# Optimization experiments

Measured on AMD Instinct MI355X. Metric: run time of the kernel, lower is better.

Reference implementation:

```python
import jax, jax.numpy as jnp
import numpy as np


def cosine_noise_schedule(t):
    # legacy mode: 1 - cos(t/1.008 * pi/2)^2
    return 1.0 - jnp.cos(t / 1.008 * jnp.pi / 2.0) ** 2


def setup_inputs() -> dict:
    key = jax.random.key(0)
    k1, k2, k3 = jax.random.split(key, 3)
    x = jax.random.normal(k1, (256, 3, 32, 32), dtype=jnp.float32)
    images = jax.random.normal(k2, (50000, 3, 32, 32), dtype=jnp.float32)
    t = jax.random.uniform(k3, (1,), dtype=jnp.float32)
    return {"t": t, "x": x, "images": images}


def reference(t, x, images):
    # Exact ideal score: softmax over dataset of Gaussian kernel weights.
    # The original streams dataset batches with an online-softmax running max;
    # with uniform batch sizes that is mathematically a global softmax over N:
    #   score = -(x - at * E_p[y]) / bt^2,  p_j = softmax(-||x - at*y_j||^2 / (2 bt^2))
    sched = cosine_noise_schedule(t)          # [1]
    bt = jnp.sqrt(sched)                      # [1]
    at = jnp.sqrt(1.0 - sched)                # [1]
    b, c, h, w = x.shape
    n = images.shape[0]
    xf = x.reshape(b, -1)                     # [b, chw]
    yf = images.reshape(n, -1)                # [n, chw]
    # ||x - at*y||^2 = ||x||^2 + at^2 ||y||^2 - 2 at x.y  (GEMM-dominant)
    x2 = jnp.sum(xf * xf, axis=1)             # [b]
    y2 = jnp.sum(yf * yf, axis=1)             # [n]
    cross = xf @ yf.T                         # [b, n]
    d2 = x2[:, None] + (at ** 2) * y2[None, :] - 2.0 * at * cross  # [b, n]
    logits = -d2 / (2.0 * bt ** 2)            # [b, n]
    p = jax.nn.softmax(logits, axis=1)        # [b, n], stable (max-subtracted)
    ybar = (p @ yf).reshape(b, c, h, w)       # softmax-weighted dataset mean
    return -(x - at * ybar) / (bt ** 2)
```

## Files before the change

kernel.cpp:

```cpp
#include <hip/hip_runtime.h>

typedef float    f32x4  __attribute__((ext_vector_type(4)));
typedef float    f32x16 __attribute__((ext_vector_type(16)));
typedef _Float16 f16x4  __attribute__((ext_vector_type(4)));
typedef _Float16 f16x8  __attribute__((ext_vector_type(8)));

#define N_IMG 50000
#define NPAD  50176
#define BROWS 256
#define CHW   3072
#define BK    64
#define BM    128
#define BN    128
#define EHS   50176
#define KCHUNK 3136
#define NSPLIT 16

__device__ __forceinline__ void glds16(const void* g, void* l) {
    __builtin_amdgcn_global_load_lds(
        (const __attribute__((address_space(1))) void*)g,
        (__attribute__((address_space(3))) void*)l, 16, 0, 0);
}

__global__ void k_scalars(const float* __restrict__ t, float* __restrict__ sc) {
    if (threadIdx.x == 0) {
        double tv  = (double)t[0];
        double ang = tv * (1.5707963267948966 / 1.008);
        double c   = cos(ang);
        double at  = c;
        double bt2 = 1.0 - c * c;
        sc[0] = (float)at;
        sc[1] = (float)bt2;
        sc[2] = (float)(at / bt2);
        sc[3] = (float)(at * at * 0.5 / bt2);
        sc[4] = (float)(1.0 / bt2);
    }
}

__global__ void k_xprep(const float* __restrict__ x, _Float16* __restrict__ xh) {
    int idx = blockIdx.x * 256 + threadIdx.x;
    f32x4 v = ((const f32x4*)x)[idx];
    f16x4 h;
    h[0] = (_Float16)v[0]; h[1] = (_Float16)v[1];
    h[2] = (_Float16)v[2]; h[3] = (_Float16)v[3];
    ((f16x4*)xh)[idx] = h;
}

__global__ void k_prep(const float* __restrict__ img, _Float16* __restrict__ imgh,
                       float* __restrict__ y2) {
    int row = blockIdx.x, tid = threadIdx.x;
    f16x4* dst = (f16x4*)(imgh + (size_t)row * CHW);
    if (row >= N_IMG) {
        f16x4 z = {(_Float16)0.f, (_Float16)0.f, (_Float16)0.f, (_Float16)0.f};
        #pragma unroll
        for (int i = 0; i < 3; i++) dst[tid + i * 256] = z;
        return;
    }
    const f32x4* src = (const f32x4*)(img + (size_t)row * CHW);
    float s = 0.f;
    #pragma unroll
    for (int i = 0; i < 3; i++) {
        f32x4 v = src[tid + i * 256];
        s += v[0]*v[0] + v[1]*v[1] + v[2]*v[2] + v[3]*v[3];
        f16x4 h;
        h[0] = (_Float16)v[0]; h[1] = (_Float16)v[1];
        h[2] = (_Float16)v[2]; h[3] = (_Float16)v[3];
        dst[tid + i * 256] = h;
    }
    for (int o = 32; o > 0; o >>= 1) s += __shfl_down(s, o);
    __shared__ float wsum[4];
    if ((tid & 63) == 0) wsum[tid >> 6] = s;
    __syncthreads();
    if (tid == 0) y2[row] = (wsum[0] + wsum[1]) + (wsum[2] + wsum[3]);
}

__global__ __launch_bounds__(256, 3) void k_gemm1(
        const _Float16* __restrict__ xh, const _Float16* __restrict__ imgh,
        const float* __restrict__ y2g, const float* __restrict__ sc,
        float* __restrict__ logits) {
    __shared__ _Float16 Alds[BM * BK];
    __shared__ _Float16 Blds[BN * BK];

    const int tid = threadIdx.x;
    const int wid = tid >> 6, lane = tid & 63;
    const int flat = blockIdx.x;
    const int xcd = flat & 7, loc = flat >> 3;
    const int m0 = (loc & 1) * BM;
    const int n0 = (xcd * 49 + (loc >> 1)) * BN;

    const _Float16* gA[4]; const _Float16* gB[4];
    _Float16* lA[4]; _Float16* lB[4];
    #pragma unroll
    for (int j = 0; j < 4; j++) {
        int seg = wid * 4 + j;
        int row = seg * 8 + (lane >> 3);
        int off = (((lane & 7) ^ (row & 7)) << 3);
        gA[j] = xh + (size_t)(m0 + row) * CHW + off;
        int rb = n0 + row; if (rb > N_IMG - 1) rb = N_IMG - 1;
        gB[j] = imgh + (size_t)rb * CHW + off;
        lA[j] = Alds + seg * 512;
        lB[j] = Blds + seg * 512;
    }

    const int wm = wid >> 1, wn = wid & 1;
    const int rm = wm * 64, cn = wn * 64;
    const int lr = lane & 31, hi = lane >> 5;
    const int xm = (lr & 7) << 4;
    const char* Ab = (const char*)Alds;
    const char* Bb = (const char*)Blds;
    const int ar0 = (rm + lr) * 128,      ar1 = (rm + 32 + lr) * 128;
    const int br0 = (cn + lr) * 128,      br1 = (cn + 32 + lr) * 128;
    const int kof = hi * 16;

    f32x16 acc[2][2];
    #pragma unroll
    for (int mi = 0; mi < 2; mi++)
        #pragma unroll
        for (int ni = 0; ni < 2; ni++)
            #pragma unroll
            for (int r = 0; r < 16; r++) acc[mi][ni][r] = 0.f;

    for (int it = 0; it < CHW / BK; ++it) {
        if (it) __syncthreads();
        #pragma unroll
        for (int j = 0; j < 4; j++) glds16(gA[j] + it * BK, lA[j]);
        #pragma unroll
        for (int j = 0; j < 4; j++) glds16(gB[j] + it * BK, lB[j]);
        __syncthreads();
        #pragma unroll
        for (int ks = 0; ks < 4; ++ks) {
            int off = (ks * 32 + kof) ^ xm;
            f16x8 a0 = *(const f16x8*)(Ab + ar0 + off);
            f16x8 a1 = *(const f16x8*)(Ab + ar1 + off);
            f16x8 b0 = *(const f16x8*)(Bb + br0 + off);
            f16x8 b1 = *(const f16x8*)(Bb + br1 + off);
            acc[0][0] = __builtin_amdgcn_mfma_f32_32x32x16_f16(a0, b0, acc[0][0], 0, 0, 0);
            acc[0][1] = __builtin_amdgcn_mfma_f32_32x32x16_f16(a0, b1, acc[0][1], 0, 0, 0);
            acc[1][0] = __builtin_amdgcn_mfma_f32_32x32x16_f16(a1, b0, acc[1][0], 0, 0, 0);
            acc[1][1] = __builtin_amdgcn_mfma_f32_32x32x16_f16(a1, b1, acc[1][1], 0, 0, 0);
        }
    }

    const float c_cross = sc[2], c_y2 = sc[3];
    #pragma unroll
    for (int mi = 0; mi < 2; mi++)
        #pragma unroll
        for (int ni = 0; ni < 2; ni++) {
            int col = n0 + cn + ni * 32 + lr;
            if (col >= N_IMG) continue;
            float y2v = y2g[col];
            f32x16 v = acc[mi][ni];
            #pragma unroll
            for (int r = 0; r < 16; r++) {
                int row = m0 + rm + mi * 32 + (r & 3) + 8 * (r >> 2) + 4 * hi;
                logits[(size_t)row * N_IMG + col] = c_cross * v[r] - c_y2 * y2v;
            }
        }
}

__global__ void k_softmax(const float* __restrict__ logits, _Float16* __restrict__ eh,
                          float* __restrict__ rowsum) {
    int row = blockIdx.x, tid = threadIdx.x;
    const f32x4* lr = (const f32x4*)(logits + (size_t)row * N_IMG);
    _Float16* erow = eh + (size_t)row * EHS;
    f16x4* er = (f16x4*)erow;
    __shared__ float wred[4];

    if (tid < EHS - N_IMG) erow[N_IMG + tid] = (_Float16)0.f;

    float m = -3.0e38f;
    for (int i = tid; i < N_IMG / 4; i += 256) {
        f32x4 v = lr[i];
        m = fmaxf(m, fmaxf(fmaxf(v[0], v[1]), fmaxf(v[2], v[3])));
    }
    for (int o = 32; o > 0; o >>= 1) m = fmaxf(m, __shfl_down(m, o));
    if ((tid & 63) == 0) wred[tid >> 6] = m;
    __syncthreads();
    m = fmaxf(fmaxf(wred[0], wred[1]), fmaxf(wred[2], wred[3]));
    __syncthreads();

    float s = 0.f;
    for (int i = tid; i < N_IMG / 4; i += 256) {
        f32x4 v = lr[i];
        float e0 = __expf(v[0] - m), e1 = __expf(v[1] - m);
        float e2 = __expf(v[2] - m), e3 = __expf(v[3] - m);
        s += (e0 + e1) + (e2 + e3);
        f16x4 h;
        h[0] = (_Float16)e0; h[1] = (_Float16)e1;
        h[2] = (_Float16)e2; h[3] = (_Float16)e3;
        er[i] = h;
    }
    for (int o = 32; o > 0; o >>= 1) s += __shfl_down(s, o);
    if ((tid & 63) == 0) wred[tid >> 6] = s;
    __syncthreads();
    if (tid == 0) rowsum[row] = (wred[0] + wred[1]) + (wred[2] + wred[3]);
}

__global__ __launch_bounds__(256, 3) void k_gemm2(
        const _Float16* __restrict__ eh, const _Float16* __restrict__ imgh,
        float* __restrict__ partial) {
    __shared__ _Float16 Alds[BM * BK];
    __shared__ _Float16 Blds[BN * BK];
    __shared__ _Float16 Tmp[BK * BN];

    const int tid = threadIdx.x;
    const int wid = tid >> 6, lane = tid & 63;
    const int flat = blockIdx.x;
    const int xcd = flat & 7, loc = flat >> 3;
    const int ck  = xcd * 2 + (loc >= 48 ? 1 : 0);
    const int rem = loc - (loc >= 48 ? 48 : 0);
    const int m0 = (rem & 1) * BM;
    const int d0 = (rem >> 1) * BN;
    const int kbase = ck * KCHUNK;

    const _Float16* gA[4]; _Float16* lA[4];
    const _Float16* gB[4]; _Float16* lB[4];
    #pragma unroll
    for (int j = 0; j < 4; j++) {
        int seg = wid * 4 + j;
        int row = seg * 8 + (lane >> 3);
        int off = (((lane & 7) ^ (row & 7)) << 3);
        gA[j] = eh + (size_t)(m0 + row) * EHS + kbase + off;
        lA[j] = Alds + seg * 512;
        gB[j] = imgh + (size_t)(kbase + seg * 4 + (lane >> 4)) * CHW + d0 + (lane & 15) * 8;
        lB[j] = Tmp + seg * 512;
    }

    const int q   = tid & 31;
    const int oct = tid >> 5;

    const int wm = wid >> 1, wn = wid & 1;
    const int rm = wm * 64, cn = wn * 64;
    const int lr = lane & 31, hi = lane >> 5;
    const int xm = (lr & 7) << 4;
    const int ar0 = (rm + lr) * 128, ar1 = (rm + 32 + lr) * 128;
    const int br0 = (cn + lr) * 128, br1 = (cn + 32 + lr) * 128;
    const int kof = hi * 16;
    const char* Ab = (const char*)Alds;
    const char* Bb = (const char*)Blds;

    f32x16 acc[2][2];
    #pragma unroll
    for (int mi = 0; mi < 2; mi++)
        #pragma unroll
        for (int ni = 0; ni < 2; ni++)
            #pragma unroll
            for (int r = 0; r < 16; r++) acc[mi][ni][r] = 0.f;

    #pragma unroll
    for (int j = 0; j < 4; j++) glds16(gA[j], lA[j]);
    #pragma unroll
    for (int j = 0; j < 4; j++) glds16(gB[j], lB[j]);

    f16x8 afr0[4], afr1[4];

    for (int it = 0; it < KCHUNK / BK; ++it) {
        __syncthreads();

        #pragma unroll
        for (int ks = 0; ks < 4; ++ks) {
            int offa = (ks * 32 + kof) ^ xm;
            afr0[ks] = *(const f16x8*)(Ab + ar0 + offa);
            afr1[ks] = *(const f16x8*)(Ab + ar1 + offa);
        }
        {
            f16x4 r[8];
            #pragma unroll
            for (int j = 0; j < 8; j++)
                r[j] = *(const f16x4*)&Tmp[(oct * 8 + j) * 128 + q * 4];
            #pragma unroll
            for (int dd = 0; dd < 4; dd++) {
                f16x8 w;
                #pragma unroll
                for (int j = 0; j < 8; j++) w[j] = r[j][dd];
                int d = q * 4 + dd;
                *(f16x8*)((char*)Blds + d * 128 + ((oct ^ (d & 7)) << 4)) = w;
            }
        }
        __syncthreads();

        if (it + 1 < KCHUNK / BK) {
            #pragma unroll
            for (int j = 0; j < 4; j++) glds16(gA[j] + (it + 1) * BK, lA[j]);
            #pragma unroll
            for (int j = 0; j < 4; j++) glds16(gB[j] + (size_t)(it + 1) * BK * CHW, lB[j]);
        }
        #pragma unroll
        for (int ks = 0; ks < 4; ++ks) {
            int offb = (ks * 32 + kof) ^ xm;
            f16x8 b0 = *(const f16x8*)(Bb + br0 + offb);
            f16x8 b1 = *(const f16x8*)(Bb + br1 + offb);
            acc[0][0] = __builtin_amdgcn_mfma_f32_32x32x16_f16(afr0[ks], b0, acc[0][0], 0, 0, 0);
            acc[0][1] = __builtin_amdgcn_mfma_f32_32x32x16_f16(afr0[ks], b1, acc[0][1], 0, 0, 0);
            acc[1][0] = __builtin_amdgcn_mfma_f32_32x32x16_f16(afr1[ks], b0, acc[1][0], 0, 0, 0);
            acc[1][1] = __builtin_amdgcn_mfma_f32_32x32x16_f16(afr1[ks], b1, acc[1][1], 0, 0, 0);
        }
    }

    float* pp = partial + (size_t)ck * BROWS * CHW;
    #pragma unroll
    for (int mi = 0; mi < 2; mi++)
        #pragma unroll
        for (int ni = 0; ni < 2; ni++) {
            int dcol = d0 + cn + ni * 32 + lr;
            f32x16 v = acc[mi][ni];
            #pragma unroll
            for (int r = 0; r < 16; r++) {
                int row = m0 + rm + mi * 32 + (r & 3) + 8 * (r >> 2) + 4 * hi;
                pp[(size_t)row * CHW + dcol] = v[r];
            }
        }
}

__global__ void k_final(const float* __restrict__ partial, const float* __restrict__ x,
                        const float* __restrict__ rowsum, const float* __restrict__ sc,
                        float* __restrict__ out) {
    int idx = blockIdx.x * 256 + threadIdx.x;
    int row = idx / (CHW / 4);
    float at = sc[0], invbt2 = sc[4];
    float scale = at * invbt2 / rowsum[row];
    const f32x4* p4 = (const f32x4*)partial;
    f32x4 s = p4[idx];
    #pragma unroll
    for (int c = 1; c < NSPLIT; c++) s = s + p4[(size_t)c * (BROWS * CHW / 4) + idx];
    f32x4 xv = ((const f32x4*)x)[idx];
    f32x4 o;
    #pragma unroll
    for (int j = 0; j < 4; j++) o[j] = s[j] * scale - xv[j] * invbt2;
    ((f32x4*)out)[idx] = o;
}

extern "C" void kernel_launch(void* const* d_in, const int* in_sizes, int n_in,
                              void* d_out, int out_size, void* d_ws, size_t ws_size,
                              hipStream_t stream) {
    const float* t   = (const float*)d_in[0];
    const float* x   = (const float*)d_in[1];
    const float* img = (const float*)d_in[2];
    float* out = (float*)d_out;
    char* ws = (char*)d_ws;

    float*    sc     = (float*)(ws + 0);
    float*    rowsum = (float*)(ws + 256);
    float*    y2     = (float*)(ws + 4096);
    _Float16* xh     = (_Float16*)(ws + 212992);
    _Float16* imgh   = (_Float16*)(ws + 2097152);
    _Float16* eh     = (_Float16*)(ws + 310378496);
    float*    logits = (float*)(ws + 336068608);
    float*    partial = logits;

    k_scalars<<<1, 64, 0, stream>>>(t, sc);
    k_xprep<<<(BROWS * CHW / 4) / 256, 256, 0, stream>>>(x, xh);
    k_prep<<<NPAD, 256, 0, stream>>>(img, imgh, y2);
    k_gemm1<<<784, 256, 0, stream>>>(xh, imgh, y2, sc, logits);
    k_softmax<<<256, 256, 0, stream>>>(logits, eh, rowsum);
    k_gemm2<<<768, 256, 0, stream>>>(eh, imgh, partial);
    k_final<<<(BROWS * CHW / 4) / 256, 256, 0, stream>>>(partial, x, rowsum, sc, out);
}
```

Measured before the change: 481.2 us.

## Fuse image fp16 conversion and squared-norm into first GEMM

```diff
diff --git a/kernel.cpp b/kernel.cpp
--- a/kernel.cpp
+++ b/kernel.cpp
@@ -46,40 +46,13 @@
     ((f16x4*)xh)[idx] = h;
 }
 
-__global__ void k_prep(const float* __restrict__ img, _Float16* __restrict__ imgh,
-                       float* __restrict__ y2) {
-    int row = blockIdx.x, tid = threadIdx.x;
-    f16x4* dst = (f16x4*)(imgh + (size_t)row * CHW);
-    if (row >= N_IMG) {
-        f16x4 z = {(_Float16)0.f, (_Float16)0.f, (_Float16)0.f, (_Float16)0.f};
-        #pragma unroll
-        for (int i = 0; i < 3; i++) dst[tid + i * 256] = z;
-        return;
-    }
-    const f32x4* src = (const f32x4*)(img + (size_t)row * CHW);
-    float s = 0.f;
-    #pragma unroll
-    for (int i = 0; i < 3; i++) {
-        f32x4 v = src[tid + i * 256];
-        s += v[0]*v[0] + v[1]*v[1] + v[2]*v[2] + v[3]*v[3];
-        f16x4 h;
-        h[0] = (_Float16)v[0]; h[1] = (_Float16)v[1];
-        h[2] = (_Float16)v[2]; h[3] = (_Float16)v[3];
-        dst[tid + i * 256] = h;
-    }
-    for (int o = 32; o > 0; o >>= 1) s += __shfl_down(s, o);
-    __shared__ float wsum[4];
-    if ((tid & 63) == 0) wsum[tid >> 6] = s;
-    __syncthreads();
-    if (tid == 0) y2[row] = (wsum[0] + wsum[1]) + (wsum[2] + wsum[3]);
-}
-
 __global__ __launch_bounds__(256, 3) void k_gemm1(
-        const _Float16* __restrict__ xh, const _Float16* __restrict__ imgh,
-        const float* __restrict__ y2g, const float* __restrict__ sc,
+        const _Float16* __restrict__ xh, const float* __restrict__ img,
+        _Float16* __restrict__ imgh, const float* __restrict__ sc,
         float* __restrict__ logits) {
-    __shared__ _Float16 Alds[BM * BK];
+    __shared__ _Float16 Alds[2][BM * BK];
     __shared__ _Float16 Blds[BN * BK];
+    __shared__ float y2lds[BN];
 
     const int tid = threadIdx.x;
     const int wid = tid >> 6, lane = tid & 63;
@@ -88,29 +61,40 @@
     const int m0 = (loc & 1) * BM;
     const int n0 = (xcd * 49 + (loc >> 1)) * BN;
 
-    const _Float16* gA[4]; const _Float16* gB[4];
-    _Float16* lA[4]; _Float16* lB[4];
+    const _Float16* gA[4]; int lAo[4];
     #pragma unroll
     for (int j = 0; j < 4; j++) {
         int seg = wid * 4 + j;
         int row = seg * 8 + (lane >> 3);
         int off = (((lane & 7) ^ (row & 7)) << 3);
         gA[j] = xh + (size_t)(m0 + row) * CHW + off;
-        int rb = n0 + row; if (rb > N_IMG - 1) rb = N_IMG - 1;
-        gB[j] = imgh + (size_t)rb * CHW + off;
-        lA[j] = Alds + seg * 512;
-        lB[j] = Blds + seg * 512;
-    }
+        lAo[j] = seg * 512;
+    }
+
+    const int br = tid >> 1;
+    const int bh = tid & 1;
+    const int bn = n0 + br;
+    const bool bvalid = bn < N_IMG;
+    const bool bwrite = (m0 == 0);
+    const float* bsrc = img + (size_t)(bvalid ? bn : 0) * CHW + bh * 32;
+    _Float16* ihdst = imgh + (size_t)bn * CHW + bh * 32;
+    char* bld = (char*)Blds + br * 128;
+
+    f32x4 breg[8];
+    float y2p = 0.f;
+    auto loadB = [&](int kt) {
+        #pragma unroll
+        for (int i = 0; i < 8; i++) breg[i] = *(const f32x4*)(bsrc + kt + i * 4);
+    };
 
     const int wm = wid >> 1, wn = wid & 1;
     const int rm = wm * 64, cn = wn * 64;
     const int lr = lane & 31, hi = lane >> 5;
     const int xm = (lr & 7) << 4;
-    const char* Ab = (const char*)Alds;
-    const char* Bb = (const char*)Blds;
     const int ar0 = (rm + lr) * 128,      ar1 = (rm + 32 + lr) * 128;
     const int br0 = (cn + lr) * 128,      br1 = (cn + 32 + lr) * 128;
     const int kof = hi * 16;
+    const char* Bb = (const char*)Blds;
 
     f32x16 acc[2][2];
     #pragma unroll
@@ -120,13 +104,41 @@
             #pragma unroll
             for (int r = 0; r < 16; r++) acc[mi][ni][r] = 0.f;
 
+    #pragma unroll
+    for (int j = 0; j < 4; j++) glds16(gA[j], (_Float16*)Alds[0] + lAo[j]);
+    loadB(0);
+
+    int c = 0;
+    const f32x4 fz = {0.f, 0.f, 0.f, 0.f};
     for (int it = 0; it < CHW / BK; ++it) {
-        if (it) __syncthreads();
-        #pragma unroll
-        for (int j = 0; j < 4; j++) glds16(gA[j] + it * BK, lA[j]);
-        #pragma unroll
-        for (int j = 0; j < 4; j++) glds16(gB[j] + it * BK, lB[j]);
         __syncthreads();
+
+        if (!bvalid) {
+            #pragma unroll
+            for (int i = 0; i < 8; i++) breg[i] = fz;
+        }
+        #pragma unroll
+        for (int gi = 0; gi < 4; gi++) {
+            f32x4 a = breg[2 * gi], b = breg[2 * gi + 1];
+            f16x8 h;
+            #pragma unroll
+            for (int q = 0; q < 4; q++) {
+                h[q]     = (_Float16)a[q];
+                h[4 + q] = (_Float16)b[q];
+                y2p += a[q] * a[q] + b[q] * b[q];
+            }
+            *(f16x8*)(bld + (((bh * 4 + gi) ^ (br & 7)) << 4)) = h;
+            if (bwrite) *(f16x8*)(ihdst + it * BK + gi * 8) = h;
+        }
+        __syncthreads();
+
+        if (it + 1 < CHW / BK) {
+            #pragma unroll
+            for (int j = 0; j < 4; j++)
+                glds16(gA[j] + (it + 1) * BK, (_Float16*)Alds[c ^ 1] + lAo[j]);
+            loadB((it + 1) * BK);
+        }
+        const char* Ab = (const char*)Alds[c];
         #pragma unroll
         for (int ks = 0; ks < 4; ++ks) {
             int off = (ks * 32 + kof) ^ xm;
@@ -139,7 +151,15 @@
             acc[1][0] = __builtin_amdgcn_mfma_f32_32x32x16_f16(a1, b0, acc[1][0], 0, 0, 0);
             acc[1][1] = __builtin_amdgcn_mfma_f32_32x32x16_f16(a1, b1, acc[1][1], 0, 0, 0);
         }
-    }
+        c ^= 1;
+    }
+
+    {
+        float s = y2p;
+        s += __shfl_xor(s, 1);
+        if (bh == 0) y2lds[br] = s;
+    }
+    __syncthreads();
 
     const float c_cross = sc[2], c_y2 = sc[3];
     #pragma unroll
@@ -148,7 +168,7 @@
         for (int ni = 0; ni < 2; ni++) {
             int col = n0 + cn + ni * 32 + lr;
             if (col >= N_IMG) continue;
-            float y2v = y2g[col];
+            float y2v = y2lds[cn + ni * 32 + lr];
             f32x16 v = acc[mi][ni];
             #pragma unroll
             for (int r = 0; r < 16; r++) {
@@ -341,7 +361,6 @@
 
     float*    sc     = (float*)(ws + 0);
     float*    rowsum = (float*)(ws + 256);
-    float*    y2     = (float*)(ws + 4096);
     _Float16* xh     = (_Float16*)(ws + 212992);
     _Float16* imgh   = (_Float16*)(ws + 2097152);
     _Float16* eh     = (_Float16*)(ws + 310378496);
@@ -350,8 +369,7 @@
 
     k_scalars<<<1, 64, 0, stream>>>(t, sc);
     k_xprep<<<(BROWS * CHW / 4) / 256, 256, 0, stream>>>(x, xh);
-    k_prep<<<NPAD, 256, 0, stream>>>(img, imgh, y2);
-    k_gemm1<<<784, 256, 0, stream>>>(xh, imgh, y2, sc, logits);
+    k_gemm1<<<784, 256, 0, stream>>>(xh, img, imgh, sc, logits);
     k_softmax<<<256, 256, 0, stream>>>(logits, eh, rowsum);
     k_gemm2<<<768, 256, 0, stream>>>(eh, imgh, partial);
     k_final<<<(BROWS * CHW / 4) / 256, 256, 0, stream>>>(partial, x, rowsum, sc, out);
```

Result: slower. 608.8 us (+26.5%).
